# Kernel tuning notes

Hardware: AMD Instinct MI355X
Metric: run time of the kernel (lower is better)

The kernel has to match this reference:

```python
import jax, jax.numpy as jnp
import numpy as np

B, P, Q, D = 16, 4096, 1024, 256


def setup_inputs() -> dict:
    key = jax.random.key(0)
    k1, k2, k3, k4 = jax.random.split(key, 4)
    return {
        "passage_encodes": jax.random.normal(k1, (B, P, D), dtype=jnp.float32),
        "question_encodes": jax.random.normal(k2, (B, Q, D), dtype=jnp.float32),
        "w_attn": jax.random.normal(k3, (2 * D, 1), dtype=jnp.float32) * (1.0 / np.sqrt(2 * D)),
        "b_attn": jnp.zeros((1,), dtype=jnp.float32),
        "w_out": jax.random.normal(k4, (2 * D, 256), dtype=jnp.float32) * (1.0 / np.sqrt(2 * D)),
        "b_out": jnp.zeros((256,), dtype=jnp.float32),
    }


def reference(passage_encodes, question_encodes, w_attn, b_attn, w_out, b_out):
    # similarity matrix [B, P, Q]
    sim = jnp.einsum('bpd,bqd->bpq', passage_encodes, question_encodes)
    # context-to-question attention
    c2q = jax.nn.softmax(sim, axis=-1)                       # [B, P, Q]
    ctx2q = jnp.einsum('bpq,bqd->bpd', c2q, question_encodes)  # [B, P, D]
    # question-to-context attention (softmax over row-max)
    q2c = jax.nn.softmax(jnp.max(sim, axis=-1), axis=-1)     # [B, P]
    q2c_vec = jnp.einsum('bp,bpd->bd', q2c, passage_encodes)  # [B, D]
    tp = jnp.tanh(passage_encodes)
    concat = jnp.concatenate([
        tp * jnp.tanh(ctx2q),
        tp * jnp.tanh(q2c_vec)[:, None, :],  # broadcast instead of repeat
    ], axis=-1)                                              # [B, P, 2D]
    # attention reducer: linear -> softmax over sequence -> weighted sum
    w = jax.nn.softmax(jnp.einsum('bpc,co->bp', concat, w_attn) + b_attn[0], axis=1)
    reduced = jnp.einsum('bp,bpc->bc', w, concat)            # [B, 2D]
    return reduced @ w_out + b_out                            # [B, output_dim]
```

## Files before the change

### kernel.cpp

```cpp
#include <hip/hip_runtime.h>
#include <cmath>

#define BB 16
#define PP 4096
#define QQ 1024
#define DD 256

typedef __attribute__((ext_vector_type(8))) short short8;
typedef __attribute__((ext_vector_type(4))) float floatx4;
typedef __attribute__((ext_vector_type(4))) _Float16 half4;

static __device__ inline ushort bf16_rne(float x) {
  unsigned u = __float_as_uint(x);
  unsigned r = (u + 0x7fffu + ((u >> 16) & 1u)) >> 16;
  return (ushort)r;
}
static __device__ inline float bf16f(ushort h) { return __uint_as_float(((unsigned)h) << 16); }

static __device__ inline float ftanh(float x) {
  float e = __expf(2.0f * x);
  return 1.0f - 2.0f * __builtin_amdgcn_rcpf(e + 1.0f);
}

static __device__ inline void gl16(const void* g, void* l) {
  __builtin_amdgcn_global_load_lds(
      (const __attribute__((address_space(1))) unsigned int*)g,
      (__attribute__((address_space(3))) unsigned int*)l, 16, 0, 0);
}

__global__ __launch_bounds__(256) void kQprep(
    const float* __restrict__ ques, ushort* __restrict__ qb)
{
  const int b = blockIdx.y, qt = blockIdx.x;
  __shared__ float tile[32][260];
  const int tid = threadIdx.x;
  const float* src = ques + ((size_t)b * QQ + qt * 32) * DD;
  for (int i = tid; i < 32 * 64; i += 256) {
    int r = i >> 6, c = (i & 63) << 2;
    *(float4*)&tile[r][c] = *(const float4*)(src + r * DD + c);
  }
  __syncthreads();
  ushort* blob = qb + (size_t)(b * 32 + qt) * 24576;
  {
    int r = tid >> 3;
    int j0 = (tid & 7) * 4;
#pragma unroll
    for (int jj = 0; jj < 4; ++jj) {
      int j = j0 + jj;
      ushort h8[8], l8[8];
#pragma unroll
      for (int e = 0; e < 8; ++e) {
        float x = tile[r][j * 8 + e];
        ushort h = bf16_rne(x);
        h8[e] = h; l8[e] = bf16_rne(x - bf16f(h));
      }
      int g = r * 32 + (j ^ (r & 7));
      *(uint4*)&blob[(size_t)g * 8] = *(uint4*)h8;
      *(uint4*)&blob[8192 + (size_t)g * 8] = *(uint4*)l8;
    }
  }
  {
    int d = tid;
    int s = (d >> 1) & 3;
    ushort h32[32];
#pragma unroll
    for (int r = 0; r < 32; ++r) h32[r] = bf16_rne(tile[r][d]);
#pragma unroll
    for (int k = 0; k < 4; ++k)
      *(uint4*)&blob[16384 + (size_t)d * 32 + (k ^ s) * 8] = *(uint4*)&h32[k * 8];
  }
}

__global__ __launch_bounds__(512, 1) void kA(
    const float* __restrict__ pass, const ushort* __restrict__ qb,
    const float* __restrict__ w_attn,
    _Float16* __restrict__ first_h, _Float16* __restrict__ tp_h,
    float* __restrict__ logit1,
    float* __restrict__ numpart, float* __restrict__ denpart)
{
  __shared__ alignas(16) char sm[147456];

  const int b    = blockIdx.y;
  const int p0   = blockIdx.x * 128;
  const int tid  = threadIdx.x;
  const int w    = tid >> 6;
  const int lane = tid & 63;
  const int l15  = lane & 15;
  const int quad = lane >> 4;
  const int swz  = l15 & 7;

  short8 bhi[8], blo[8];
  {
    const float* prow = pass + (((size_t)b * PP + p0 + w * 16 + l15) * DD);
#pragma unroll
    for (int c = 0; c < 8; ++c) {
      const float* p8 = prow + c * 32 + quad * 8;
      float4 x0 = *(const float4*)p8;
      float4 x1 = *(const float4*)(p8 + 4);
      float xs[8] = {x0.x, x0.y, x0.z, x0.w, x1.x, x1.y, x1.z, x1.w};
#pragma unroll
      for (int j = 0; j < 8; ++j) {
        ushort h = bf16_rne(xs[j]);
        ushort lo = bf16_rne(xs[j] - bf16f(h));
        bhi[c][j] = (short)h;
        blo[c][j] = (short)lo;
      }
    }
  }

  int goff[8];
#pragma unroll
  for (int c = 0; c < 8; ++c) goff[c] = (l15 * 32 + ((4 * c + quad) ^ swz)) * 8;
  const int vtoff = l15 * 32 + ((quad ^ ((l15 >> 1) & 3)) * 8);

  const ushort* tb = qb + (size_t)b * 32 * 24576;
  const int dma_l = w * 3072 + lane * 8;
  const int dma_s = w * 6144 + lane * 16;

  floatx4 accO[16];
#pragma unroll
  for (int i = 0; i < 16; ++i) accO[i] = (floatx4){0.f, 0.f, 0.f, 0.f};
  float mx = -INFINITY, ps = 0.f;
  short8 phi = {0, 0, 0, 0, 0, 0, 0, 0}, plo = {0, 0, 0, 0, 0, 0, 0, 0};

  {
    const ushort* gs = tb + dma_l;
    char* ld = sm + dma_s;
#pragma unroll
    for (int i = 0; i < 6; ++i) gl16(gs + i * 512, ld + i * 1024);
  }
  __syncthreads();

  for (int t = 0; t < 32; ++t) {
    const int ic = t % 3, ip = (t + 2) % 3, inx = (t + 1) % 3;
    char* cur = sm + ic * 49152;
    char* prv = sm + ip * 49152;
    if (t < 31) {
      const ushort* gs = tb + (size_t)(t + 1) * 24576 + dma_l;
      char* ld = sm + inx * 49152 + dma_s;
#pragma unroll
      for (int i = 0; i < 6; ++i) gl16(gs + i * 512, ld + i * 1024);
    }

    const ushort* Qhi = (const ushort*)cur;
    const ushort* Qlo = (const ushort*)(cur + 16384);
    floatx4 s0 = (floatx4){0.f, 0.f, 0.f, 0.f};
    floatx4 s1 = (floatx4){0.f, 0.f, 0.f, 0.f};
#pragma unroll
    for (int c = 0; c < 8; ++c) {
      short8 a0h = *(const short8*)&Qhi[goff[c]];
      short8 a0l = *(const short8*)&Qlo[goff[c]];
      short8 a1h = *(const short8*)&Qhi[goff[c] + 4096];
      short8 a1l = *(const short8*)&Qlo[goff[c] + 4096];
      s0 = __builtin_amdgcn_mfma_f32_16x16x32_bf16(a0h, bhi[c], s0, 0, 0, 0);
      s0 = __builtin_amdgcn_mfma_f32_16x16x32_bf16(a0h, blo[c], s0, 0, 0, 0);
      s0 = __builtin_amdgcn_mfma_f32_16x16x32_bf16(a0l, bhi[c], s0, 0, 0, 0);
      s1 = __builtin_amdgcn_mfma_f32_16x16x32_bf16(a1h, bhi[c], s1, 0, 0, 0);
      s1 = __builtin_amdgcn_mfma_f32_16x16x32_bf16(a1h, blo[c], s1, 0, 0, 0);
      s1 = __builtin_amdgcn_mfma_f32_16x16x32_bf16(a1l, bhi[c], s1, 0, 0, 0);
    }

    if (t > 0) {
      const ushort* TQ = (const ushort*)(prv + 32768);
#pragma unroll
      for (int nt = 0; nt < 16; ++nt) {
        short8 vhi = *(const short8*)&TQ[nt * 512 + vtoff];
        accO[nt] = __builtin_amdgcn_mfma_f32_16x16x32_bf16(phi, vhi, accO[nt], 0, 0, 0);
        accO[nt] = __builtin_amdgcn_mfma_f32_16x16x32_bf16(plo, vhi, accO[nt], 0, 0, 0);
      }
    }

    float pv[8];
#pragma unroll
    for (int r = 0; r < 4; ++r) {
      float s = s0[r];
      mx = fmaxf(mx, s);
      pv[r] = __expf(s - 60.f);
      ps += pv[r];
    }
#pragma unroll
    for (int r = 0; r < 4; ++r) {
      float s = s1[r];
      mx = fmaxf(mx, s);
      pv[4 + r] = __expf(s - 60.f);
      ps += pv[4 + r];
    }

    unsigned* pwv = (unsigned*)prv + w * 512;
#pragma unroll
    for (int mt = 0; mt < 2; ++mt) {
      unsigned pk[4];
#pragma unroll
      for (int r = 0; r < 4; ++r) {
        float x = pv[mt * 4 + r];
        ushort h = bf16_rne(x);
        ushort lo = bf16_rne(x - bf16f(h));
        pk[r] = (unsigned)h | ((unsigned)lo << 16);
      }
      int g = l15 * 8 + ((mt * 4 + quad) ^ swz);
      *(uint4*)&pwv[g * 4] = *(uint4*)pk;
    }
    uint4 u0 = *(const uint4*)&pwv[(l15 * 8 + ((2 * quad) ^ swz)) * 4];
    uint4 u1 = *(const uint4*)&pwv[(l15 * 8 + ((2 * quad + 1) ^ swz)) * 4];
    unsigned ua[8] = {u0.x, u0.y, u0.z, u0.w, u1.x, u1.y, u1.z, u1.w};
#pragma unroll
    for (int j = 0; j < 8; ++j) {
      phi[j] = (short)(ua[j] & 0xffffu);
      plo[j] = (short)(ua[j] >> 16);
    }
    __syncthreads();
  }

  {
    const ushort* TQ = (const ushort*)(sm + 49152 + 32768);
#pragma unroll
    for (int nt = 0; nt < 16; ++nt) {
      short8 vhi = *(const short8*)&TQ[nt * 512 + vtoff];
      accO[nt] = __builtin_amdgcn_mfma_f32_16x16x32_bf16(phi, vhi, accO[nt], 0, 0, 0);
      accO[nt] = __builtin_amdgcn_mfma_f32_16x16x32_bf16(plo, vhi, accO[nt], 0, 0, 0);
    }
  }

  ps += __shfl_xor(ps, 16);
  ps += __shfl_xor(ps, 32);
  mx = fmaxf(mx, __shfl_xor(mx, 16));
  mx = fmaxf(mx, __shfl_xor(mx, 32));

  __syncthreads();
  float* Of = (float*)(sm + w * 16640);
#pragma unroll
  for (int nt = 0; nt < 16; ++nt)
#pragma unroll
    for (int r = 0; r < 4; ++r)
      Of[(quad * 4 + r) * 260 + nt * 16 + l15] = accO[nt][r];
  const float4 w1 = *(const float4*)(w_attn + lane * 4);
  const size_t rowoff = (size_t)b * PP + p0 + w * 16;
  float4 qacc = make_float4(0.f, 0.f, 0.f, 0.f);
  float dacc = 0.f;
#pragma unroll
  for (int j = 0; j < 16; ++j) {
    float4 o = *(const float4*)&Of[j * 260 + lane * 4];
    float linv = 1.f / __shfl(ps, j);
    float4 pv4 = *(const float4*)(pass + (rowoff + j) * DD + lane * 4);
    float wj = __expf(__shfl(mx, j) - 60.f);
    qacc.x += wj * pv4.x; qacc.y += wj * pv4.y;
    qacc.z += wj * pv4.z; qacc.w += wj * pv4.w;
    dacc += wj;
    float tpx = ftanh(pv4.x), tpy = ftanh(pv4.y), tpz = ftanh(pv4.z), tpw = ftanh(pv4.w);
    float4 f;
    f.x = tpx * ftanh(o.x * linv);
    f.y = tpy * ftanh(o.y * linv);
    f.z = tpz * ftanh(o.z * linv);
    f.w = tpw * ftanh(o.w * linv);
    half4 fh = {(_Float16)f.x, (_Float16)f.y, (_Float16)f.z, (_Float16)f.w};
    half4 th = {(_Float16)tpx, (_Float16)tpy, (_Float16)tpz, (_Float16)tpw};
    *(half4*)(first_h + (rowoff + j) * DD + lane * 4) = fh;
    *(half4*)(tp_h + (rowoff + j) * DD + lane * 4) = th;
    float part = f.x * w1.x + f.y * w1.y + f.z * w1.z + f.w * w1.w;
    part += __shfl_xor(part, 1);  part += __shfl_xor(part, 2);
    part += __shfl_xor(part, 4);  part += __shfl_xor(part, 8);
    part += __shfl_xor(part, 16); part += __shfl_xor(part, 32);
    if (lane == 0) logit1[rowoff + j] = part;
  }

  float* redw = (float*)(sm + w * 16640);
  *(float4*)&redw[lane * 4] = qacc;
  if (lane == 0) redw[256] = dacc;
  __syncthreads();
  if (w == 0) {
    float4 s = make_float4(0.f, 0.f, 0.f, 0.f);
    float dsum = 0.f;
#pragma unroll
    for (int wv = 0; wv < 8; ++wv) {
      const float* rp = (const float*)(sm + wv * 16640);
      float4 v = *(const float4*)&rp[lane * 4];
      s.x += v.x; s.y += v.y; s.z += v.z; s.w += v.w;
      dsum += rp[256];
    }
    *(float4*)(numpart + (size_t)(blockIdx.x * 16 + b) * DD + lane * 4) = s;
    if (lane == 0) denpart[blockIdx.x * 16 + b] = dsum;
  }
}

__global__ __launch_bounds__(256) void kE(
    const _Float16* __restrict__ tp_h, const _Float16* __restrict__ first_h,
    const float* __restrict__ logit1,
    const float* __restrict__ numpart, const float* __restrict__ denpart,
    const float* __restrict__ w_attn,
    float* __restrict__ r1part, float* __restrict__ r2part, float* __restrict__ den2part)
{
  const int b = blockIdx.y, chunk = blockIdx.x;
  const int tid = threadIdx.x, r = tid >> 6, ln = tid & 63;
  __shared__ float s1[4][64][4];
  __shared__ float s2[4][64][4];
  __shared__ float sd[4][64];
  __shared__ alignas(16) float w2s[256];
  {
    float num = 0.f, den = 0.f;
#pragma unroll
    for (int c = 0; c < 32; ++c) {
      num += numpart[(size_t)(c * 16 + b) * DD + tid];
      den += denpart[c * 16 + b];
    }
    w2s[tid] = w_attn[DD + tid] * ftanh(num / den);
  }
  __syncthreads();
  const float4 wv = *(const float4*)&w2s[ln << 2];
  const float* lg = logit1 + (size_t)b * PP + chunk * 64;
  const size_t base = ((size_t)b * PP + chunk * 64) * DD;
  float a1[4] = {0.f, 0.f, 0.f, 0.f}, a2[4] = {0.f, 0.f, 0.f, 0.f};
  float den = 0.f;
  for (int p = r; p < 64; p += 4) {
    half4 f = *(const half4*)(first_h + base + (size_t)p * DD + ln * 4);
    half4 t = *(const half4*)(tp_h + base + (size_t)p * DD + ln * 4);
    float part = (float)t.x * wv.x + (float)t.y * wv.y +
                 (float)t.z * wv.z + (float)t.w * wv.w;
    part += __shfl_xor(part, 1);  part += __shfl_xor(part, 2);
    part += __shfl_xor(part, 4);  part += __shfl_xor(part, 8);
    part += __shfl_xor(part, 16); part += __shfl_xor(part, 32);
    float wgt = __expf(lg[p] + part);
    a1[0] += wgt * (float)f.x; a1[1] += wgt * (float)f.y;
    a1[2] += wgt * (float)f.z; a1[3] += wgt * (float)f.w;
    a2[0] += wgt * (float)t.x; a2[1] += wgt * (float)t.y;
    a2[2] += wgt * (float)t.z; a2[3] += wgt * (float)t.w;
    den += wgt;
  }
  *(float4*)&s1[r][ln][0] = *(float4*)a1;
  *(float4*)&s2[r][ln][0] = *(float4*)a2;
  sd[r][ln] = den;
  __syncthreads();
  if (r == 0) {
    float o1[4], o2[4];
#pragma unroll
    for (int i = 0; i < 4; ++i) {
      o1[i] = s1[0][ln][i] + s1[1][ln][i] + s1[2][ln][i] + s1[3][ln][i];
      o2[i] = s2[0][ln][i] + s2[1][ln][i] + s2[2][ln][i] + s2[3][ln][i];
    }
    *(float4*)(r1part + (size_t)(chunk * 16 + b) * DD + ln * 4) = *(float4*)o1;
    *(float4*)(r2part + (size_t)(chunk * 16 + b) * DD + ln * 4) = *(float4*)o2;
    if (ln == 0)
      den2part[chunk * 16 + b] = sd[0][0] + sd[1][0] + sd[2][0] + sd[3][0];
  }
}

__global__ __launch_bounds__(256) void kF(
    const float* __restrict__ r1part, const float* __restrict__ r2part,
    const float* __restrict__ den2part,
    const float* __restrict__ numpart, const float* __restrict__ denpart,
    const float* __restrict__ w_out, const float* __restrict__ b_out,
    float* __restrict__ out)
{
  const int b = blockIdx.x >> 2, og = blockIdx.x & 3;
  const int tid = threadIdx.x;
  __shared__ alignas(16) float R1[256], R2[256];
  __shared__ float sacc[4][64];
  {
    float red1 = 0.f, red2 = 0.f, den2 = 0.f;
#pragma unroll
    for (int c = 0; c < 64; ++c) {
      red1 += r1part[(size_t)(c * 16 + b) * DD + tid];
      red2 += r2part[(size_t)(c * 16 + b) * DD + tid];
      den2 += den2part[c * 16 + b];
    }
    float num = 0.f, den = 0.f;
#pragma unroll
    for (int c = 0; c < 32; ++c) {
      num += numpart[(size_t)(c * 16 + b) * DD + tid];
      den += denpart[c * 16 + b];
    }
    float t = ftanh(num / den);
    float inv = 1.f / den2;
    R1[tid] = red1 * inv;
    R2[tid] = red2 * inv * t;
  }
  __syncthreads();
  const int oi = tid & 63, ks = tid >> 6;
  const int o = og * 64 + oi;
  float acc = 0.f;
  for (int k = ks * 64; k < ks * 64 + 64; ++k) {
    acc += R1[k] * w_out[k * 256 + o];
    acc += R2[k] * w_out[(DD + k) * 256 + o];
  }
  sacc[ks][oi] = acc;
  __syncthreads();
  if (ks == 0) {
    float v = sacc[0][oi] + sacc[1][oi] + sacc[2][oi] + sacc[3][oi];
    out[b * 256 + o] = v + b_out[o];
  }
}

extern "C" void kernel_launch(void* const* d_in, const int* in_sizes, int n_in,
                              void* d_out, int out_size, void* d_ws, size_t ws_size,
                              hipStream_t stream) {
  const float* pass   = (const float*)d_in[0];
  const float* ques   = (const float*)d_in[1];
  const float* w_attn = (const float*)d_in[2];
  const float* w_out  = (const float*)d_in[4];
  const float* b_out  = (const float*)d_in[5];
  float* out = (float*)d_out;

  float* ws       = (float*)d_ws;
  float* logit1   = ws;
  float* numpart  = logit1   + (size_t)BB * PP;
  float* denpart  = numpart  + (size_t)32 * BB * DD;
  float* r1part   = denpart  + 32 * BB;
  float* r2part   = r1part   + (size_t)64 * BB * DD;
  float* den2part = r2part   + (size_t)64 * BB * DD;
  ushort* qbb     = (ushort*)(den2part + 64 * BB);
  _Float16* first_h = (_Float16*)(qbb + (size_t)BB * 32 * 24576);
  _Float16* tp_h    = first_h + (size_t)BB * PP * DD;

  kQprep<<<dim3(QQ / 32, BB), 256, 0, stream>>>(ques, qbb);
  kA    <<<dim3(PP / 128, BB), 512, 0, stream>>>(pass, qbb, w_attn,
                                                 first_h, tp_h, logit1,
                                                 numpart, denpart);
  kE    <<<dim3(64, BB), 256, 0, stream>>>(tp_h, first_h, logit1,
                                           numpart, denpart, w_attn,
                                           r1part, r2part, den2part);
  kF    <<<64, 256, 0, stream>>>(r1part, r2part, den2part,
                                 numpart, denpart, w_out, b_out, out);
}
```

Before: 327.4 us.

## Permute transposed Q blob so P fragments stay in registers without LDS shuffle

Changes the element ordering of the transposed bf16 question tile in the blob, interleaving groups of four rows. This lets the softmax probability fragments from the S MFMA output feed the PV MFMA directly from registers. It removes the per-iteration LDS write/read round trip that repacked P into MFMA operand layout. Correctness depends on the k-index permutation matching between the P register layout and the V layout.

After: 320.9 us. 1.02x faster.

```diff
diff --git a/kernel.cpp b/kernel.cpp
--- a/kernel.cpp
+++ b/kernel.cpp
@@ -66,8 +66,15 @@
 #pragma unroll
     for (int r = 0; r < 32; ++r) h32[r] = bf16_rne(tile[r][d]);
 #pragma unroll
-    for (int k = 0; k < 4; ++k)
-      *(uint4*)&blob[16384 + (size_t)d * 32 + (k ^ s) * 8] = *(uint4*)&h32[k * 8];
+    for (int k = 0; k < 4; ++k) {
+      ushort g8[8];
+#pragma unroll
+      for (int e = 0; e < 4; ++e) {
+        g8[e]     = h32[k * 4 + e];
+        g8[4 + e] = h32[16 + k * 4 + e];
+      }
+      *(uint4*)&blob[16384 + (size_t)d * 32 + (k ^ s) * 8] = *(uint4*)g8;
+    }
   }
 }
 
@@ -170,43 +177,30 @@
       }
     }
 
-    float pv[8];
-#pragma unroll
-    for (int r = 0; r < 4; ++r) {
-      float s = s0[r];
-      mx = fmaxf(mx, s);
-      pv[r] = __expf(s - 60.f);
-      ps += pv[r];
-    }
-#pragma unroll
-    for (int r = 0; r < 4; ++r) {
-      float s = s1[r];
-      mx = fmaxf(mx, s);
-      pv[4 + r] = __expf(s - 60.f);
-      ps += pv[4 + r];
-    }
-
-    unsigned* pwv = (unsigned*)prv + w * 512;
-#pragma unroll
-    for (int mt = 0; mt < 2; ++mt) {
-      unsigned pk[4];
+    {
+      short8 nph, npl;
 #pragma unroll
       for (int r = 0; r < 4; ++r) {
-        float x = pv[mt * 4 + r];
+        float s = s0[r];
+        mx = fmaxf(mx, s);
+        float x = __expf(s - 60.f);
+        ps += x;
         ushort h = bf16_rne(x);
-        ushort lo = bf16_rne(x - bf16f(h));
-        pk[r] = (unsigned)h | ((unsigned)lo << 16);
-      }
-      int g = l15 * 8 + ((mt * 4 + quad) ^ swz);
-      *(uint4*)&pwv[g * 4] = *(uint4*)pk;
-    }
-    uint4 u0 = *(const uint4*)&pwv[(l15 * 8 + ((2 * quad) ^ swz)) * 4];
-    uint4 u1 = *(const uint4*)&pwv[(l15 * 8 + ((2 * quad + 1) ^ swz)) * 4];
-    unsigned ua[8] = {u0.x, u0.y, u0.z, u0.w, u1.x, u1.y, u1.z, u1.w};
-#pragma unroll
-    for (int j = 0; j < 8; ++j) {
-      phi[j] = (short)(ua[j] & 0xffffu);
-      plo[j] = (short)(ua[j] >> 16);
+        nph[r] = (short)h;
+        npl[r] = (short)bf16_rne(x - bf16f(h));
+      }
+#pragma unroll
+      for (int r = 0; r < 4; ++r) {
+        float s = s1[r];
+        mx = fmaxf(mx, s);
+        float x = __expf(s - 60.f);
+        ps += x;
+        ushort h = bf16_rne(x);
+        nph[4 + r] = (short)h;
+        npl[4 + r] = (short)bf16_rne(x - bf16f(h));
+      }
+      phi = nph;
+      plo = npl;
     }
     __syncthreads();
   }
```
